# Optimization experiments

Measured on AMD Instinct MI355X. Metric: run time of the kernel, lower is better.

## Reference

```python
import jax, jax.numpy as jnp
import numpy as np

EMBED = 1024
HEADS = 16
HEAD_DIM = EMBED // HEADS          # 64
POS_DIM = 256
POS_PER_HEAD = POS_DIM // HEADS    # 16
POS_IDX = 64
N, L = 8, 1024


def setup_inputs() -> dict:
    key = jax.random.key(0)
    ks = jax.random.split(key, 10)
    s = 0.02
    return {
        "values": jax.random.normal(ks[0], (N, L, EMBED), jnp.float32),
        "keys": jax.random.normal(ks[1], (N, L, EMBED), jnp.float32),
        "query": jax.random.normal(ks[2], (N, L, EMBED), jnp.float32),
        "position": jax.random.normal(ks[3], (N, L, POS_IDX), jnp.float32),
        # torch Linear weights: shape (out_features, in_features)
        "Wv": jax.random.normal(ks[4], (HEAD_DIM, HEAD_DIM), jnp.float32) * s,
        "Wk": jax.random.normal(ks[5], (HEAD_DIM, HEAD_DIM), jnp.float32) * s,
        "Wq": jax.random.normal(ks[6], (HEAD_DIM, HEAD_DIM + POS_PER_HEAD), jnp.float32) * s,
        "Wpos": jax.random.normal(ks[7], (POS_DIM, POS_IDX), jnp.float32) * s,
        "Wo": jax.random.normal(ks[8], (EMBED, EMBED), jnp.float32) * s,
        "bo": jax.random.normal(ks[9], (EMBED,), jnp.float32) * s,
    }


def reference(values, keys, query, position, Wv, Wk, Wq, Wpos, Wo, bo):
    n, qlen = query.shape[0], query.shape[1]
    vlen, klen = values.shape[1], keys.shape[1]
    # position embedding: Linear(pos_idx -> pos_dim)
    pos_emb = position @ Wpos.T                                   # [N, q, POS_DIM]
    q_with_pos = jnp.concatenate([query, pos_emb], axis=2)        # [N, q, EMBED+POS_DIM]
    # split heads
    v = values.reshape(n, vlen, HEADS, HEAD_DIM)
    k = keys.reshape(n, klen, HEADS, HEAD_DIM)
    qp = q_with_pos.reshape(n, qlen, HEADS, HEAD_DIM + POS_PER_HEAD)
    # per-head linear projections (no bias)
    v = jnp.einsum('nlhd,ed->nlhe', v, Wv)
    k = jnp.einsum('nlhd,ed->nlhe', k, Wk)
    q = jnp.einsum('nqhd,ed->nqhe', qp, Wq)
    # attention: note scale uses sqrt(embed_size), as in the original
    energy = jnp.einsum('nqhd,nkhd->nhqk', q, k)
    attn = jax.nn.softmax(energy / jnp.sqrt(jnp.asarray(EMBED, energy.dtype)), axis=3)
    out = jnp.einsum('nhql,nlhd->nqhd', attn, v).reshape(n, qlen, EMBED)
    return out @ Wo.T + bo
```

## Files before the change

kernel.cpp:

```cpp
#include <hip/hip_runtime.h>
#include <hip/hip_bf16.h>


typedef __hip_bfloat16 bf16;
typedef unsigned int u32;
typedef unsigned short u16;
typedef short short8 __attribute__((ext_vector_type(8)));
typedef float f32x4 __attribute__((ext_vector_type(4)));
typedef float f32x16 __attribute__((ext_vector_type(16)));
typedef unsigned int u32x2 __attribute__((ext_vector_type(2)));

#define MFMA16(a, b, c) __builtin_amdgcn_mfma_f32_16x16x32_bf16((a), (b), (c), 0, 0, 0)
#define MFMA32(a, b, c) __builtin_amdgcn_mfma_f32_32x32x16_bf16((a), (b), (c), 0, 0, 0)

#define QSCALE 0.04508422002777998f

__device__ __forceinline__ short8 ld8(const bf16* p) { return *(const short8*)p; }

__device__ __forceinline__ u32 pk2(float a, float b) {
  u16 ua = __bfloat16_as_ushort(__float2bfloat16(a));
  u16 ub = __bfloat16_as_ushort(__float2bfloat16(b));
  return (u32)ua | ((u32)ub << 16);
}

__device__ __forceinline__ float fexp2(float x) {
  float r;
  asm("v_exp_f32 %0, %1" : "=v"(r) : "v"(x));
  return r;
}

__device__ __forceinline__ u32 cvtpk(float a, float b) {
  u32 r;
  asm("v_cvt_pk_bf16_f32 %0, %1, %2" : "=v"(r) : "v"(a), "v"(b));
  return r;
}

__device__ __forceinline__ void gload16(const void* g, void* l) {
  __builtin_amdgcn_global_load_lds(
      (const __attribute__((address_space(1))) u32*)g,
      (__attribute__((address_space(3))) u32*)l, 16, 0, 0);
}

union S8U { short8 s; u32 u[4]; };

__device__ __forceinline__ short8 ld8f(const float* p) {
  float4 a = ((const float4*)p)[0];
  float4 b = ((const float4*)p)[1];
  S8U r;
  r.u[0] = pk2(a.x, a.y);
  r.u[1] = pk2(a.z, a.w);
  r.u[2] = pk2(b.x, b.y);
  r.u[3] = pk2(b.z, b.w);
  return r.s;
}

__global__ __launch_bounds__(256) void cvt_wo(const float* __restrict__ w,
                                              bf16* __restrict__ o) {
  int i = blockIdx.x * 256 + threadIdx.x;
  o[i] = __float2bfloat16(w[i]);
}

__global__ __launch_bounds__(256) void pos_gemm(const float* __restrict__ position,
                                                const float* __restrict__ Wpos,
                                                bf16* __restrict__ posb) {
  const int t = threadIdx.x;
  const int lane = t & 63, wave = t >> 6;
  const int g = lane >> 4, c = lane & 15;
  const int wr = wave >> 1, wc = wave & 1;
  const int r0 = blockIdx.x * 128 + wr * 64;
  const int c0 = blockIdx.y * 128 + wc * 64;
  f32x4 acc[4][4];
#pragma unroll
  for (int ai = 0; ai < 4; ++ai)
#pragma unroll
    for (int bi = 0; bi < 4; ++bi) acc[ai][bi] = (f32x4){0.f, 0.f, 0.f, 0.f};
#pragma unroll
  for (int k0 = 0; k0 < 64; k0 += 32) {
    short8 af[4], bfr[4];
#pragma unroll
    for (int ai = 0; ai < 4; ++ai)
      af[ai] = ld8f(position + (size_t)(r0 + ai * 16 + c) * 64 + k0 + 8 * g);
#pragma unroll
    for (int bi = 0; bi < 4; ++bi)
      bfr[bi] = ld8f(Wpos + (size_t)(c0 + bi * 16 + c) * 64 + k0 + 8 * g);
#pragma unroll
    for (int ai = 0; ai < 4; ++ai)
#pragma unroll
      for (int bi = 0; bi < 4; ++bi) acc[ai][bi] = MFMA16(af[ai], bfr[bi], acc[ai][bi]);
  }
#pragma unroll
  for (int bi = 0; bi < 4; ++bi) {
    const int p = c0 + bi * 16 + c;
#pragma unroll
    for (int ai = 0; ai < 4; ++ai) {
#pragma unroll
      for (int i = 0; i < 4; ++i) {
        int row = r0 + ai * 16 + 4 * g + i;
        posb[(size_t)row * 256 + p] = __float2bfloat16(acc[ai][bi][i]);
      }
    }
  }
}

__global__ __launch_bounds__(256) void k_gemm(const float* __restrict__ src,
                                              const float* __restrict__ W,
                                              bf16* __restrict__ dst) {
  const int t = threadIdx.x;
  const int lane = t & 63, wave = t >> 6;
  const int g = lane >> 4, c = lane & 15;
  const int wr = wave >> 1, wc = wave & 1;
  const int r0 = blockIdx.x * 128 + wr * 64;
  const int c0 = wc * 32;
  const int h = blockIdx.y;
  f32x4 acc[4][2];
#pragma unroll
  for (int ai = 0; ai < 4; ++ai)
#pragma unroll
    for (int bi = 0; bi < 2; ++bi) acc[ai][bi] = (f32x4){0.f, 0.f, 0.f, 0.f};
#pragma unroll
  for (int k0 = 0; k0 < 64; k0 += 32) {
    short8 af[4], bfr[2];
#pragma unroll
    for (int ai = 0; ai < 4; ++ai)
      af[ai] = ld8f(src + (size_t)(r0 + ai * 16 + c) * 1024 + 64 * h + k0 + 8 * g);
#pragma unroll
    for (int bi = 0; bi < 2; ++bi)
      bfr[bi] = ld8f(W + (size_t)(c0 + bi * 16 + c) * 64 + k0 + 8 * g);
#pragma unroll
    for (int ai = 0; ai < 4; ++ai)
#pragma unroll
      for (int bi = 0; bi < 2; ++bi) acc[ai][bi] = MFMA16(af[ai], bfr[bi], acc[ai][bi]);
  }
#pragma unroll
  for (int bi = 0; bi < 2; ++bi) {
    const int e = c0 + bi * 16 + c;
#pragma unroll
    for (int ai = 0; ai < 4; ++ai) {
#pragma unroll
      for (int i = 0; i < 4; ++i) {
        int row = r0 + ai * 16 + 4 * g + i;
        int n = row >> 10, l = row & 1023;
        dst[(((size_t)(n * 16 + h)) * 1024 + l) * 64 + e] = __float2bfloat16(acc[ai][bi][i]);
      }
    }
  }
}

__global__ __launch_bounds__(256) void v_gemm(const float* __restrict__ src,
                                              const float* __restrict__ W,
                                              bf16* __restrict__ vT) {
  __shared__ __align__(16) char tlds[64 * 272];
  const int t = threadIdx.x;
  const int lane = t & 63, wave = t >> 6;
  const int g = lane >> 4, c = lane & 15;
  const int wr = wave >> 1, wc = wave & 1;
  const int r0 = blockIdx.x * 128 + wr * 64;
  const int c0 = wc * 32;
  const int h = blockIdx.y;
  f32x4 acc[4][2];
#pragma unroll
  for (int ai = 0; ai < 4; ++ai)
#pragma unroll
    for (int bi = 0; bi < 2; ++bi) acc[ai][bi] = (f32x4){0.f, 0.f, 0.f, 0.f};
#pragma unroll
  for (int k0 = 0; k0 < 64; k0 += 32) {
    short8 af[4], bfr[2];
#pragma unroll
    for (int ai = 0; ai < 4; ++ai)
      af[ai] = ld8f(src + (size_t)(r0 + ai * 16 + c) * 1024 + 64 * h + k0 + 8 * g);
#pragma unroll
    for (int bi = 0; bi < 2; ++bi)
      bfr[bi] = ld8f(W + (size_t)(c0 + bi * 16 + c) * 64 + k0 + 8 * g);
#pragma unroll
    for (int ai = 0; ai < 4; ++ai)
#pragma unroll
      for (int bi = 0; bi < 2; ++bi) acc[ai][bi] = MFMA16(af[ai], bfr[bi], acc[ai][bi]);
  }
#pragma unroll
  for (int bi = 0; bi < 2; ++bi) {
    const int e_loc = c0 + bi * 16 + c;
#pragma unroll
    for (int ai = 0; ai < 4; ++ai) {
      const int l0 = wr * 64 + ai * 16 + 4 * g;
      *(u32*)(tlds + e_loc * 272 + l0 * 2) = pk2(acc[ai][bi][0], acc[ai][bi][1]);
      *(u32*)(tlds + e_loc * 272 + l0 * 2 + 4) = pk2(acc[ai][bi][2], acc[ai][bi][3]);
    }
  }
  __syncthreads();
  const int n = blockIdx.x >> 3;
  const int lglob0 = (blockIdx.x & 7) * 128;
  bf16* vbase = vT + ((size_t)(n * 16 + h)) * 64 * 1024;
#pragma unroll
  for (int j = 0; j < 4; ++j) {
    const int id = t + j * 256;
    const int e = id >> 4, lc = (id & 15) * 8;
    *(short8*)(vbase + (size_t)e * 1024 + lglob0 + lc) =
        *(const short8*)(tlds + e * 272 + lc * 2);
  }
}

__global__ __launch_bounds__(256) void q_gemm(const float* __restrict__ query,
                                              const bf16* __restrict__ posb,
                                              const float* __restrict__ Wq,
                                              bf16* __restrict__ qb) {
  const int t = threadIdx.x;
  const int lane = t & 63, wave = t >> 6;
  const int g = lane >> 4, c = lane & 15;
  const int wr = wave >> 1, wc = wave & 1;
  const int r0 = blockIdx.x * 128 + wr * 64;
  const int c0 = wc * 32;
  const int h = blockIdx.y;
  f32x4 acc[4][2];
#pragma unroll
  for (int ai = 0; ai < 4; ++ai)
#pragma unroll
    for (int bi = 0; bi < 2; ++bi) acc[ai][bi] = (f32x4){0.f, 0.f, 0.f, 0.f};
  const short8 z8 = (short8){0, 0, 0, 0, 0, 0, 0, 0};
#pragma unroll
  for (int k0 = 0; k0 < 80; k0 += 32) {
    const bool tail_dead = (k0 == 64) && (g >= 2);
    const int col = 80 * h + k0 + 8 * g;
    short8 af[4], bfr[2];
#pragma unroll
    for (int ai = 0; ai < 4; ++ai) {
      const int row = r0 + ai * 16 + c;
      af[ai] = tail_dead ? z8
               : (col < 1024 ? ld8f(query + (size_t)row * 1024 + col)
                             : ld8(posb + (size_t)row * 256 + (col - 1024)));
    }
#pragma unroll
    for (int bi = 0; bi < 2; ++bi)
      bfr[bi] = tail_dead ? z8
                          : ld8f(Wq + (size_t)(c0 + bi * 16 + c) * 80 + k0 + 8 * g);
#pragma unroll
    for (int ai = 0; ai < 4; ++ai)
#pragma unroll
      for (int bi = 0; bi < 2; ++bi) acc[ai][bi] = MFMA16(af[ai], bfr[bi], acc[ai][bi]);
  }
#pragma unroll
  for (int bi = 0; bi < 2; ++bi) {
    const int e = c0 + bi * 16 + c;
#pragma unroll
    for (int ai = 0; ai < 4; ++ai) {
#pragma unroll
      for (int i = 0; i < 4; ++i) {
        int row = r0 + ai * 16 + 4 * g + i;
        int n = row >> 10, l = row & 1023;
        qb[(((size_t)(n * 16 + h)) * 1024 + l) * 64 + e] =
            __float2bfloat16(acc[ai][bi][i] * QSCALE);
      }
    }
  }
}

__global__ __launch_bounds__(512) void attn_kernel(const bf16* __restrict__ qb,
                                                   const bf16* __restrict__ kb,
                                                   const bf16* __restrict__ vT,
                                                   bf16* __restrict__ ob) {
  __shared__ __align__(16) char smem[2][16384];
  const int t = threadIdx.x;
  const int lane = t & 63, wave = t >> 6;
  const int l31 = lane & 31, hi = lane >> 5;
  const int qt = blockIdx.x, h = blockIdx.y, n = blockIdx.z;
  const int nh = n * 16 + h;
  const int q0 = qt * 256 + wave * 32;

  const bf16* kpan = kb + (size_t)nh * 1024 * 64;
  const bf16* vpan = vT + (size_t)nh * 64 * 1024;

  const int srow = (wave << 3) + (lane >> 3);
  const int scg = (lane & 7) ^ (srow & 7);
  const bf16* kg0 = kpan + ((size_t)srow << 6) + (scg << 3);
  const bf16* vg0 = vpan + ((size_t)srow << 10) + (scg << 3);

  const bf16* qrow = qb + ((size_t)nh * 1024 + q0 + l31) * 64 + 8 * hi;
  short8 qf[4];
#pragma unroll
  for (int ds = 0; ds < 4; ++ds) qf[ds] = ld8(qrow + ds * 16);

  f32x16 acc0, acc1;
#pragma unroll
  for (int r = 0; r < 16; ++r) {
    acc0[r] = 0.f;
    acc1[r] = 0.f;
  }
  float l_run = 0.f;

  gload16(kg0, smem[0] + wave * 1024);
  gload16(vg0, smem[0] + 8192 + wave * 1024);
  __syncthreads();

  int cur = 0;
  for (int kt = 0; kt < 16; ++kt) {
    if (kt < 15) {
      gload16(kg0 + (size_t)(kt + 1) * 64 * 64, smem[cur ^ 1] + wave * 1024);
      gload16(vg0 + (kt + 1) * 64, smem[cur ^ 1] + 8192 + wave * 1024);
    }
    const char* kt_ = smem[cur];
    const char* vt_ = smem[cur] + 8192;

#pragma unroll
    for (int s = 0; s < 2; ++s) {
      const int kr = s * 32 + l31;
      short8 kf[4], vf[2][2];
#pragma unroll
      for (int ds = 0; ds < 4; ++ds)
        kf[ds] = *(const short8*)(kt_ + kr * 128 + (((2 * ds + hi) ^ (kr & 7)) << 4));
#pragma unroll
      for (int dt = 0; dt < 2; ++dt) {
        const int vr = dt * 32 + l31;
#pragma unroll
        for (int ks = 0; ks < 2; ++ks)
          vf[dt][ks] = *(const short8*)(
              vt_ + vr * 128 + (((s * 4 + ks * 2 + hi) ^ (vr & 7)) << 4));
      }

      f32x16 sr;
#pragma unroll
      for (int r = 0; r < 16; ++r) sr[r] = 0.f;
      __builtin_amdgcn_s_setprio(1);
      sr = MFMA32(kf[0], qf[0], sr);
      sr = MFMA32(kf[1], qf[1], sr);
      sr = MFMA32(kf[2], qf[2], sr);
      sr = MFMA32(kf[3], qf[3], sr);
      __builtin_amdgcn_s_setprio(0);

      float p[16];
#pragma unroll
      for (int r = 0; r < 16; ++r) p[r] = fexp2(sr[r]);

      u32 c01 = cvtpk(p[0], p[1]), c23 = cvtpk(p[2], p[3]);
      u32 c45 = cvtpk(p[4], p[5]), c67 = cvtpk(p[6], p[7]);
      u32 c89 = cvtpk(p[8], p[9]), cab = cvtpk(p[10], p[11]);
      u32 ccd = cvtpk(p[12], p[13]), cef = cvtpk(p[14], p[15]);
      u32x2 s0a = __builtin_amdgcn_permlane32_swap(c01, c45, false, false);
      u32x2 s0b = __builtin_amdgcn_permlane32_swap(c23, c67, false, false);
      u32x2 s1a = __builtin_amdgcn_permlane32_swap(c89, ccd, false, false);
      u32x2 s1b = __builtin_amdgcn_permlane32_swap(cab, cef, false, false);
      S8U pf0, pf1;
      pf0.u[0] = s0a[0];
      pf0.u[1] = s0b[0];
      pf0.u[2] = s0a[1];
      pf0.u[3] = s0b[1];
      pf1.u[0] = s1a[0];
      pf1.u[1] = s1b[0];
      pf1.u[2] = s1a[1];
      pf1.u[3] = s1b[1];

      __builtin_amdgcn_s_setprio(1);
      acc0 = MFMA32(vf[0][0], pf0.s, acc0);
      acc0 = MFMA32(vf[0][1], pf1.s, acc0);
      acc1 = MFMA32(vf[1][0], pf0.s, acc1);
      acc1 = MFMA32(vf[1][1], pf1.s, acc1);
      __builtin_amdgcn_s_setprio(0);

      float s01 = p[0] + p[1], s23 = p[2] + p[3], s45 = p[4] + p[5];
      float s67 = p[6] + p[7], s89 = p[8] + p[9], sab = p[10] + p[11];
      float scd = p[12] + p[13], sef = p[14] + p[15];
      float ps = ((s01 + s23) + (s45 + s67)) + ((s89 + sab) + (scd + sef));
      ps += __shfl_xor(ps, 32);
      l_run += ps;
    }
    __syncthreads();
    cur ^= 1;
  }

  const float inv = 1.f / l_run;
  bf16* obase = ob + ((size_t)(n * 1024 + q0 + l31) * 16 + h) * 64;
#pragma unroll
  for (int dt = 0; dt < 2; ++dt) {
#pragma unroll
    for (int rb = 0; rb < 4; ++rb) {
      const int d0 = dt * 32 + rb * 8 + 4 * hi;
      const f32x16& a = dt ? acc1 : acc0;
      u32x2 w;
      w[0] = pk2(a[4 * rb + 0] * inv, a[4 * rb + 1] * inv);
      w[1] = pk2(a[4 * rb + 2] * inv, a[4 * rb + 3] * inv);
      *(u32x2*)(obase + d0) = w;
    }
  }
}

__global__ __launch_bounds__(256) void out_gemm(const bf16* __restrict__ A,
                                                const bf16* __restrict__ B,
                                                const float* __restrict__ bias,
                                                float* __restrict__ out) {
  __shared__ __align__(16) char smem[2][16384];
  const int t = threadIdx.x;
  const int lane = t & 63, wave = t >> 6;
  const int g = lane >> 4, c = lane & 15;
  const int wr = wave >> 1, wc = wave & 1;
  const int r0 = blockIdx.y * 128;
  const int c0 = blockIdx.x * 128;

  const int srow = t >> 2;
  const int scg = (t & 3) ^ ((srow >> 1) & 3);
  const bf16* ag0 = A + (size_t)(r0 + srow) * 1024 + scg * 8;
  const bf16* ag1 = A + (size_t)(r0 + 64 + srow) * 1024 + scg * 8;
  const bf16* bg0 = B + (size_t)(c0 + srow) * 1024 + scg * 8;
  const bf16* bg1 = B + (size_t)(c0 + 64 + srow) * 1024 + scg * 8;

  f32x4 acc[4][4];
#pragma unroll
  for (int ai = 0; ai < 4; ++ai)
#pragma unroll
    for (int bi = 0; bi < 4; ++bi) acc[ai][bi] = (f32x4){0.f, 0.f, 0.f, 0.f};

  const int wb = wave * 1024;

  {
    char* s0 = smem[0];
    gload16(ag0, s0 + wb);
    gload16(ag1, s0 + 4096 + wb);
    gload16(bg0, s0 + 8192 + wb);
    gload16(bg1, s0 + 12288 + wb);
  }
  __syncthreads();

  int cur = 0;
  for (int kt = 0; kt < 32; ++kt) {
    if (kt < 31) {
      const int k1 = (kt + 1) * 32;
      char* sn = smem[cur ^ 1];
      gload16(ag0 + k1, sn + wb);
      gload16(ag1 + k1, sn + 4096 + wb);
      gload16(bg0 + k1, sn + 8192 + wb);
      gload16(bg1 + k1, sn + 12288 + wb);
    }
    const char* sa = smem[cur];
    const char* sb = smem[cur] + 8192;

    short8 af[4], bfr[4];
#pragma unroll
    for (int ai = 0; ai < 4; ++ai) {
      const int row = wr * 64 + ai * 16 + c;
      af[ai] = *(const short8*)(sa + row * 64 + ((g ^ ((row >> 1) & 3)) << 4));
    }
#pragma unroll
    for (int bi = 0; bi < 4; ++bi) {
      const int row = wc * 64 + bi * 16 + c;
      bfr[bi] = *(const short8*)(sb + row * 64 + ((g ^ ((row >> 1) & 3)) << 4));
    }
    __builtin_amdgcn_s_setprio(1);
#pragma unroll
    for (int ai = 0; ai < 4; ++ai)
#pragma unroll
      for (int bi = 0; bi < 4; ++bi) acc[ai][bi] = MFMA16(af[ai], bfr[bi], acc[ai][bi]);
    __builtin_amdgcn_s_setprio(0);

    __syncthreads();
    cur ^= 1;
  }

#pragma unroll
  for (int bi = 0; bi < 4; ++bi) {
    const int e = c0 + wc * 64 + bi * 16 + c;
    const float bv = bias[e];
#pragma unroll
    for (int ai = 0; ai < 4; ++ai) {
#pragma unroll
      for (int i = 0; i < 4; ++i) {
        out[(size_t)(r0 + wr * 64 + ai * 16 + 4 * g + i) * 1024 + e] =
            acc[ai][bi][i] + bv;
      }
    }
  }
}

extern "C" void kernel_launch(void* const* d_in, const int* in_sizes, int n_in,
                              void* d_out, int out_size, void* d_ws, size_t ws_size,
                              hipStream_t stream) {
  const float* values = (const float*)d_in[0];
  const float* keys = (const float*)d_in[1];
  const float* query = (const float*)d_in[2];
  const float* position = (const float*)d_in[3];
  const float* Wv = (const float*)d_in[4];
  const float* Wk = (const float*)d_in[5];
  const float* Wq = (const float*)d_in[6];
  const float* Wpos = (const float*)d_in[7];
  const float* Wo = (const float*)d_in[8];
  const float* bo = (const float*)d_in[9];

  char* ws = (char*)d_ws;
  bf16* qb = (bf16*)(ws);
  bf16* kb = (bf16*)(ws + ((size_t)16 << 20));
  bf16* vT = (bf16*)(ws + ((size_t)32 << 20));
  bf16* posb = (bf16*)(ws + ((size_t)48 << 20));
  bf16* ob = (bf16*)(ws + ((size_t)52 << 20));
  bf16* wo16 = (bf16*)(ws + ((size_t)68 << 20));
  float* out = (float*)d_out;

  cvt_wo<<<4096, 256, 0, stream>>>(Wo, wo16);
  pos_gemm<<<dim3(64, 2), 256, 0, stream>>>(position, Wpos, posb);
  k_gemm<<<dim3(64, 16), 256, 0, stream>>>(keys, Wk, kb);
  v_gemm<<<dim3(64, 16), 256, 0, stream>>>(values, Wv, vT);
  q_gemm<<<dim3(64, 16), 256, 0, stream>>>(query, posb, Wq, qb);
  attn_kernel<<<dim3(4, 16, 8), 512, 0, stream>>>(qb, kb, vT, ob);
  out_gemm<<<dim3(8, 64), 256, 0, stream>>>(ob, wo16, bo, out);
}
```

Before: 137.4 us.

## Process two 32-row query tiles per wave in attention, halving waves per block

The attention kernel now uses 4 waves per block instead of 8, and each wave handles 64 query rows as two 32-row sub-tiles that share the K and V fragments read from LDS. This halves LDS fragment reads per unit of work and gives each wave more independent MFMA chains. In exchange, register pressure roughly doubles for accumulators and scores, and each thread issues twice as many global-to-LDS loads. Latency hiding now relies on two blocks per CU via launch bounds.

```diff
diff --git a/kernel.cpp b/kernel.cpp
--- a/kernel.cpp
+++ b/kernel.cpp
@@ -253,48 +253,65 @@
   }
 }
 
-__global__ __launch_bounds__(512) void attn_kernel(const bf16* __restrict__ qb,
-                                                   const bf16* __restrict__ kb,
-                                                   const bf16* __restrict__ vT,
-                                                   bf16* __restrict__ ob) {
+__global__ __launch_bounds__(256, 2) void attn_kernel(const bf16* __restrict__ qb,
+                                                      const bf16* __restrict__ kb,
+                                                      const bf16* __restrict__ vT,
+                                                      bf16* __restrict__ ob) {
   __shared__ __align__(16) char smem[2][16384];
   const int t = threadIdx.x;
   const int lane = t & 63, wave = t >> 6;
   const int l31 = lane & 31, hi = lane >> 5;
   const int qt = blockIdx.x, h = blockIdx.y, n = blockIdx.z;
   const int nh = n * 16 + h;
-  const int q0 = qt * 256 + wave * 32;
-
-  const bf16* kpan = kb + (size_t)nh * 1024 * 64;
-  const bf16* vpan = vT + (size_t)nh * 64 * 1024;
-
-  const int srow = (wave << 3) + (lane >> 3);
-  const int scg = (lane & 7) ^ (srow & 7);
-  const bf16* kg0 = kpan + ((size_t)srow << 6) + (scg << 3);
-  const bf16* vg0 = vpan + ((size_t)srow << 10) + (scg << 3);
-
-  const bf16* qrow = qb + ((size_t)nh * 1024 + q0 + l31) * 64 + 8 * hi;
-  short8 qf[4];
-#pragma unroll
-  for (int ds = 0; ds < 4; ++ds) qf[ds] = ld8(qrow + ds * 16);
-
-  f32x16 acc0, acc1;
+  const int q0 = qt * 256 + wave * 64;
+
+  const bf16* kpan = kb + (size_t)nh * 65536;
+  const bf16* vpan = vT + (size_t)nh * 65536;
+
+  const int sr8 = lane >> 3;
+  const int scg = (lane & 7) ^ sr8;
+  const int row0 = wave * 8 + sr8;
+  const bf16* kgA = kpan + (size_t)row0 * 64 + scg * 8;
+  const bf16* kgB = kpan + (size_t)(32 + row0) * 64 + scg * 8;
+  const bf16* vgA = vpan + (size_t)row0 * 1024 + scg * 8;
+  const bf16* vgB = vpan + (size_t)(32 + row0) * 1024 + scg * 8;
+  const int ldsoff = wave * 1024;
+
+  const bf16* qrowA = qb + ((size_t)nh * 1024 + q0 + l31) * 64 + 8 * hi;
+  const bf16* qrowB = qrowA + 32 * 64;
+  short8 qfA[4], qfB[4];
+#pragma unroll
+  for (int ds = 0; ds < 4; ++ds) {
+    qfA[ds] = ld8(qrowA + ds * 16);
+    qfB[ds] = ld8(qrowB + ds * 16);
+  }
+
+  f32x16 accA0, accA1, accB0, accB1;
 #pragma unroll
   for (int r = 0; r < 16; ++r) {
-    acc0[r] = 0.f;
-    acc1[r] = 0.f;
-  }
-  float l_run = 0.f;
-
-  gload16(kg0, smem[0] + wave * 1024);
-  gload16(vg0, smem[0] + 8192 + wave * 1024);
+    accA0[r] = 0.f;
+    accA1[r] = 0.f;
+    accB0[r] = 0.f;
+    accB1[r] = 0.f;
+  }
+  float lA = 0.f, lB = 0.f;
+
+  gload16(kgA, smem[0] + ldsoff);
+  gload16(kgB, smem[0] + 4096 + ldsoff);
+  gload16(vgA, smem[0] + 8192 + ldsoff);
+  gload16(vgB, smem[0] + 12288 + ldsoff);
   __syncthreads();
 
   int cur = 0;
   for (int kt = 0; kt < 16; ++kt) {
     if (kt < 15) {
-      gload16(kg0 + (size_t)(kt + 1) * 64 * 64, smem[cur ^ 1] + wave * 1024);
-      gload16(vg0 + (kt + 1) * 64, smem[cur ^ 1] + 8192 + wave * 1024);
+      char* sn = smem[cur ^ 1];
+      const size_t ko = (size_t)(kt + 1) * 4096;
+      const int vo = (kt + 1) * 64;
+      gload16(kgA + ko, sn + ldsoff);
+      gload16(kgB + ko, sn + 4096 + ldsoff);
+      gload16(vgA + vo, sn + 8192 + ldsoff);
+      gload16(vgB + vo, sn + 12288 + ldsoff);
     }
     const char* kt_ = smem[cur];
     const char* vt_ = smem[cur] + 8192;
@@ -315,68 +332,110 @@
               vt_ + vr * 128 + (((s * 4 + ks * 2 + hi) ^ (vr & 7)) << 4));
       }
 
-      f32x16 sr;
-#pragma unroll
-      for (int r = 0; r < 16; ++r) sr[r] = 0.f;
+      f32x16 srA, srB;
+#pragma unroll
+      for (int r = 0; r < 16; ++r) {
+        srA[r] = 0.f;
+        srB[r] = 0.f;
+      }
       __builtin_amdgcn_s_setprio(1);
-      sr = MFMA32(kf[0], qf[0], sr);
-      sr = MFMA32(kf[1], qf[1], sr);
-      sr = MFMA32(kf[2], qf[2], sr);
-      sr = MFMA32(kf[3], qf[3], sr);
+      srA = MFMA32(kf[0], qfA[0], srA);
+      srA = MFMA32(kf[1], qfA[1], srA);
+      srA = MFMA32(kf[2], qfA[2], srA);
+      srA = MFMA32(kf[3], qfA[3], srA);
+      srB = MFMA32(kf[0], qfB[0], srB);
+      srB = MFMA32(kf[1], qfB[1], srB);
+      srB = MFMA32(kf[2], qfB[2], srB);
+      srB = MFMA32(kf[3], qfB[3], srB);
       __builtin_amdgcn_s_setprio(0);
 
-      float p[16];
-#pragma unroll
-      for (int r = 0; r < 16; ++r) p[r] = fexp2(sr[r]);
-
-      u32 c01 = cvtpk(p[0], p[1]), c23 = cvtpk(p[2], p[3]);
-      u32 c45 = cvtpk(p[4], p[5]), c67 = cvtpk(p[6], p[7]);
-      u32 c89 = cvtpk(p[8], p[9]), cab = cvtpk(p[10], p[11]);
-      u32 ccd = cvtpk(p[12], p[13]), cef = cvtpk(p[14], p[15]);
-      u32x2 s0a = __builtin_amdgcn_permlane32_swap(c01, c45, false, false);
-      u32x2 s0b = __builtin_amdgcn_permlane32_swap(c23, c67, false, false);
-      u32x2 s1a = __builtin_amdgcn_permlane32_swap(c89, ccd, false, false);
-      u32x2 s1b = __builtin_amdgcn_permlane32_swap(cab, cef, false, false);
-      S8U pf0, pf1;
-      pf0.u[0] = s0a[0];
-      pf0.u[1] = s0b[0];
-      pf0.u[2] = s0a[1];
-      pf0.u[3] = s0b[1];
-      pf1.u[0] = s1a[0];
-      pf1.u[1] = s1b[0];
-      pf1.u[2] = s1a[1];
-      pf1.u[3] = s1b[1];
+      float pA[16], pB[16];
+#pragma unroll
+      for (int r = 0; r < 16; ++r) pA[r] = fexp2(srA[r]);
+#pragma unroll
+      for (int r = 0; r < 16; ++r) pB[r] = fexp2(srB[r]);
+
+      u32 a01 = cvtpk(pA[0], pA[1]), a23 = cvtpk(pA[2], pA[3]);
+      u32 a45 = cvtpk(pA[4], pA[5]), a67 = cvtpk(pA[6], pA[7]);
+      u32 a89 = cvtpk(pA[8], pA[9]), aab = cvtpk(pA[10], pA[11]);
+      u32 acd = cvtpk(pA[12], pA[13]), aef = cvtpk(pA[14], pA[15]);
+      u32x2 sa0 = __builtin_amdgcn_permlane32_swap(a01, a45, false, false);
+      u32x2 sa1 = __builtin_amdgcn_permlane32_swap(a23, a67, false, false);
+      u32x2 sa2 = __builtin_amdgcn_permlane32_swap(a89, acd, false, false);
+      u32x2 sa3 = __builtin_amdgcn_permlane32_swap(aab, aef, false, false);
+      S8U pfA0, pfA1;
+      pfA0.u[0] = sa0[0];
+      pfA0.u[1] = sa1[0];
+      pfA0.u[2] = sa0[1];
+      pfA0.u[3] = sa1[1];
+      pfA1.u[0] = sa2[0];
+      pfA1.u[1] = sa3[0];
+      pfA1.u[2] = sa2[1];
+      pfA1.u[3] = sa3[1];
+
+      u32 b01 = cvtpk(pB[0], pB[1]), b23 = cvtpk(pB[2], pB[3]);
+      u32 b45 = cvtpk(pB[4], pB[5]), b67 = cvtpk(pB[6], pB[7]);
+      u32 b89 = cvtpk(pB[8], pB[9]), bab = cvtpk(pB[10], pB[11]);
+      u32 bcd = cvtpk(pB[12], pB[13]), bef = cvtpk(pB[14], pB[15]);
+      u32x2 sb0 = __builtin_amdgcn_permlane32_swap(b01, b45, false, false);
+      u32x2 sb1 = __builtin_amdgcn_permlane32_swap(b23, b67, false, false);
+      u32x2 sb2 = __builtin_amdgcn_permlane32_swap(b89, bcd, false, false);
+      u32x2 sb3 = __builtin_amdgcn_permlane32_swap(bab, bef, false, false);
+      S8U pfB0, pfB1;
+      pfB0.u[0] = sb0[0];
+      pfB0.u[1] = sb1[0];
+      pfB0.u[2] = sb0[1];
+      pfB0.u[3] = sb1[1];
+      pfB1.u[0] = sb2[0];
+      pfB1.u[1] = sb3[0];
+      pfB1.u[2] = sb2[1];
+      pfB1.u[3] = sb3[1];
 
       __builtin_amdgcn_s_setprio(1);
-      acc0 = MFMA32(vf[0][0], pf0.s, acc0);
-      acc0 = MFMA32(vf[0][1], pf1.s, acc0);
-      acc1 = MFMA32(vf[1][0], pf0.s, acc1);
-      acc1 = MFMA32(vf[1][1], pf1.s, acc1);
+      accA0 = MFMA32(vf[0][0], pfA0.s, accA0);
+      accA0 = MFMA32(vf[0][1], pfA1.s, accA0);
+      accA1 = MFMA32(vf[1][0], pfA0.s, accA1);
+      accA1 = MFMA32(vf[1][1], pfA1.s, accA1);
+      accB0 = MFMA32(vf[0][0], pfB0.s, accB0);
+      accB0 = MFMA32(vf[0][1], pfB1.s, accB0);
+      accB1 = MFMA32(vf[1][0], pfB0.s, accB1);
+      accB1 = MFMA32(vf[1][1], pfB1.s, accB1);
       __builtin_amdgcn_s_setprio(0);
 
-      float s01 = p[0] + p[1], s23 = p[2] + p[3], s45 = p[4] + p[5];
-      float s67 = p[6] + p[7], s89 = p[8] + p[9], sab = p[10] + p[11];
-      float scd = p[12] + p[13], sef = p[14] + p[15];
-      float ps = ((s01 + s23) + (s45 + s67)) + ((s89 + sab) + (scd + sef));
-      ps += __shfl_xor(ps, 32);
-      l_run += ps;
+      float psA = ((pA[0] + pA[1]) + (pA[2] + pA[3])) +
+                  ((pA[4] + pA[5]) + (pA[6] + pA[7])) +
+                  ((pA[8] + pA[9]) + (pA[10] + pA[11])) +
+                  ((pA[12] + pA[13]) + (pA[14] + pA[15]));
+      float psB = ((pB[0] + pB[1]) + (pB[2] + pB[3])) +
+                  ((pB[4] + pB[5]) + (pB[6] + pB[7])) +
+                  ((pB[8] + pB[9]) + (pB[10] + pB[11])) +
+                  ((pB[12] + pB[13]) + (pB[14] + pB[15]));
+      psA += __shfl_xor(psA, 32);
+      psB += __shfl_xor(psB, 32);
+      lA += psA;
+      lB += psB;
     }
     __syncthreads();
     cur ^= 1;
   }
 
-  const float inv = 1.f / l_run;
-  bf16* obase = ob + ((size_t)(n * 1024 + q0 + l31) * 16 + h) * 64;
+  const float invA = 1.f / lA, invB = 1.f / lB;
+  bf16* obaseA = ob + ((size_t)(n * 1024 + q0 + l31) * 16 + h) * 64;
+  bf16* obaseB = obaseA + (size_t)32 * 16 * 64;
 #pragma unroll
   for (int dt = 0; dt < 2; ++dt) {
 #pragma unroll
     for (int rb = 0; rb < 4; ++rb) {
       const int d0 = dt * 32 + rb * 8 + 4 * hi;
-      const f32x16& a = dt ? acc1 : acc0;
-      u32x2 w;
-      w[0] = pk2(a[4 * rb + 0] * inv, a[4 * rb + 1] * inv);
-      w[1] = pk2(a[4 * rb + 2] * inv, a[4 * rb + 3] * inv);
-      *(u32x2*)(obase + d0) = w;
+      const f32x16& aA = dt ? accA1 : accA0;
+      const f32x16& aB = dt ? accB1 : accB0;
+      u32x2 wA, wB;
+      wA[0] = pk2(aA[4 * rb + 0] * invA, aA[4 * rb + 1] * invA);
+      wA[1] = pk2(aA[4 * rb + 2] * invA, aA[4 * rb + 3] * invA);
+      wB[0] = pk2(aB[4 * rb + 0] * invB, aB[4 * rb + 1] * invB);
+      wB[1] = pk2(aB[4 * rb + 2] * invB, aB[4 * rb + 3] * invB);
+      *(u32x2*)(obaseA + d0) = wA;
+      *(u32x2*)(obaseB + d0) = wB;
     }
   }
 }
@@ -495,6 +554,6 @@
   k_gemm<<<dim3(64, 16), 256, 0, stream>>>(keys, Wk, kb);
   v_gemm<<<dim3(64, 16), 256, 0, stream>>>(values, Wv, vT);
   q_gemm<<<dim3(64, 16), 256, 0, stream>>>(query, posb, Wq, qb);
-  attn_kernel<<<dim3(4, 16, 8), 512, 0, stream>>>(qb, kb, vT, ob);
+  attn_kernel<<<dim3(4, 16, 8), 256, 0, stream>>>(qb, kb, vT, ob);
   out_gemm<<<dim3(8, 64), 256, 0, stream>>>(ob, wo16, bo, out);
 }
```

New measurement: 132.5 us. -3.6%, faster.
